# Optimization experiments

Hardware: AMD Instinct MI355X
Metric: run time of the kernel (lower is better)

## Reference

```python
import jax, jax.numpy as jnp
import numpy as np

B, M, EMBED, HEADS = 64, 1024, 1024, 8
HD = EMBED // HEADS  # 128
MID = 64             # att_mid_dim[1]
ALPHA = 1.3          # cfg.MODEL.BILINEAR.ELU_ALPHA (CELU)


def celu(x):
    return jax.nn.celu(x, alpha=ALPHA)


def group_norm(x, w, b, G=HEADS, eps=1e-5):
    # torch GroupNorm in source uses unbiased variance (ddof=1)
    N, C = x.shape
    xg = x.reshape(N, G, C // G)
    m = xg.mean(-1, keepdims=True)
    v = xg.var(-1, ddof=1, keepdims=True)
    xg = (xg - m) / jnp.sqrt(v + eps)
    return xg.reshape(N, C) * w + b


def setup_inputs() -> dict:
    key = jax.random.key(0)
    ks = jax.random.split(key, 16)
    s = 0.02
    return {
        "h_state": jax.random.normal(ks[0], (B, EMBED), jnp.float32),
        "att_feats": jax.random.normal(ks[1], (B, M, EMBED), jnp.float32),
        "att_mask": jnp.ones((B, M), jnp.float32),
        "p_att_feats": jax.random.normal(ks[2], (B, M, 2 * EMBED), jnp.float32),
        "Wq": jax.random.normal(ks[3], (EMBED, EMBED), jnp.float32) * s,
        "bq": jnp.zeros((EMBED,), jnp.float32),
        "gnw_q": jnp.ones((EMBED,), jnp.float32),
        "gnb_q": jnp.zeros((EMBED,), jnp.float32),
        "Wv1": jax.random.normal(ks[4], (EMBED, EMBED), jnp.float32) * s,
        "bv1": jnp.zeros((EMBED,), jnp.float32),
        "gnw_v1": jnp.ones((EMBED,), jnp.float32),
        "gnb_v1": jnp.zeros((EMBED,), jnp.float32),
        "Wb": jax.random.normal(ks[5], (HEADS, HD, MID), jnp.float32) * s,
        "bb": jax.random.normal(ks[6], (HEADS, MID), jnp.float32) * s,
        "Ws": jax.random.normal(ks[7], (HEADS, MID, 1), jnp.float32) * s,
        "bs": jax.random.normal(ks[8], (HEADS, 1), jnp.float32) * s,
        "Wc": jax.random.normal(ks[9], (HEADS, MID, HD), jnp.float32) * s,
        "bc": jax.random.normal(ks[10], (HEADS, HD), jnp.float32) * s,
        "Wt": jax.random.normal(ks[11], (2 * EMBED, EMBED), jnp.float32) * s,
        "bt": jnp.zeros((EMBED,), jnp.float32),
        "lnw": jnp.ones((EMBED,), jnp.float32),
        "lnb": jnp.zeros((EMBED,), jnp.float32),
    }


def reference(h_state, att_feats, att_mask, p_att_feats,
              Wq, bq, gnw_q, gnb_q, Wv1, bv1, gnw_v1, gnb_v1,
              Wb, bb, Ws, bs, Wc, bc, Wt, bt, lnw, lnb):
    b = h_state.shape[0]
    # precompute=True path: split p_att_feats into key / value2
    p_key = p_att_feats[..., :EMBED]
    p_value2 = p_att_feats[..., EMBED:]

    # q / v1 branches: Linear -> CELU -> GroupNorm
    q = group_norm(celu(h_state @ Wq + bq), gnw_q, gnb_q)    # [B, E]
    v1 = group_norm(celu(h_state @ Wv1 + bv1), gnw_v1, gnb_v1)

    p_query = q.reshape(b, HEADS, HD)[:, :, None, :]          # [B, H, 1, D]
    p_value1 = v1.reshape(b, HEADS, HD)[:, :, None, :]        # [B, H, 1, D]
    p_key = p_key.reshape(b, M, HEADS, HD).transpose(0, 2, 1, 3)     # [B, H, M, D]
    p_value2 = p_value2.reshape(b, M, HEADS, HD).transpose(0, 2, 1, 3)

    fusion = p_value2 * p_value1                              # [B, H, M, D]
    att_map = p_query * p_key                                 # [B, H, M, D]

    # attention_basic: MH_Linear + ReLU (dropout is identity at eval)
    am = jax.nn.relu(jnp.einsum('bhmi,hio->bhmo', att_map, Wb) + bb[None, :, None, :])  # [B,H,M,MID]

    mask = att_mask[:, None, :]                               # [B, 1, M]
    mext = mask[..., None]                                    # [B, 1, M, 1]
    att_map_pool = (am * mext).sum(-2) / mext.sum(-2)         # [B, H, MID]

    alpha_spatial = (jnp.einsum('bhmi,hio->bhmo', am, Ws) + bs[None, :, None, :])[..., 0]  # [B,H,M]
    alpha_spatial = jnp.where(mask == 0, -1e9, alpha_spatial)
    alpha_spatial = jax.nn.softmax(alpha_spatial, axis=-1)

    att = jnp.einsum('bhm,bhmd->bhd', alpha_spatial, fusion)  # [B, H, D]

    alpha_channel = jax.nn.sigmoid(jnp.einsum('bhi,hio->bho', att_map_pool, Wc) + bc[None])
    att = (att * alpha_channel).reshape(b, EMBED)

    out = jnp.concatenate([h_state, att], axis=-1) @ Wt + bt  # [B, E]
    mu = out.mean(-1, keepdims=True)
    var = out.var(-1, keepdims=True)
    out = (out - mu) / jnp.sqrt(var + 1e-5) * lnw + lnb
    return out
```

## Files before the change

### kernel.cpp

```cpp
#include <hip/hip_runtime.h>
#include <hip/hip_bf16.h>
#include <cmath>

#define NB 64
#define NM 1024
#define NE 1024
#define NH 8
#define NHD 128
#define NMID 64
#define CELU_ALPHA 1.3f

typedef __attribute__((ext_vector_type(8))) short bf16x8;
typedef __attribute__((ext_vector_type(4))) float f32x4;

__device__ __forceinline__ float celuf(float x) {
    return x > 0.f ? x : CELU_ALPHA * expm1f(x / CELU_ALPHA);
}

__device__ __forceinline__ short f2bf(float x) {
    __hip_bfloat16 b = __float2bfloat16(x);
    return *reinterpret_cast<short*>(&b);
}

__global__ __launch_bounds__(256) void a1_tile(
    const float* __restrict__ h, const float* __restrict__ Wq,
    const float* __restrict__ Wv1, float* __restrict__ partA)
{
    const int t = threadIdx.x;
    const int mat = blockIdx.x >> 7;
    const int kq = (blockIdx.x >> 4) & 7;
    const int cc = (blockIdx.x & 15) * 64;
    const int kbase = kq * 128;
    const float* __restrict__ W = mat ? Wv1 : Wq;

    __shared__ float wl[128][64];
    __shared__ float hl[64][132];

#pragma unroll
    for (int u = 0; u < 8; ++u) {
        const int f = t + 256 * u;
        const int row = f >> 4, c4 = f & 15;
        *(float4*)&wl[row][c4 * 4] =
            *(const float4*)&W[(size_t)(kbase + row) * 1024 + cc + c4 * 4];
    }
#pragma unroll
    for (int u = 0; u < 8; ++u) {
        const int f = t + 256 * u;
        const int r = f >> 5, k4 = f & 31;
        *(float4*)&hl[r][k4 * 4] = *(const float4*)&h[r * 1024 + kbase + k4 * 4];
    }
    __syncthreads();

    const int r0 = (t >> 4) * 4;
    const int c0 = (t & 15) * 4;
    float acc[4][4];
#pragma unroll
    for (int i = 0; i < 4; ++i)
#pragma unroll
        for (int j = 0; j < 4; ++j) acc[i][j] = 0.f;

#pragma unroll 4
    for (int k = 0; k < 128; ++k) {
        const float4 w4 = *(const float4*)&wl[k][c0];
        const float h0 = hl[r0][k], h1 = hl[r0 + 1][k];
        const float h2 = hl[r0 + 2][k], h3 = hl[r0 + 3][k];
        acc[0][0] = fmaf(h0, w4.x, acc[0][0]); acc[0][1] = fmaf(h0, w4.y, acc[0][1]);
        acc[0][2] = fmaf(h0, w4.z, acc[0][2]); acc[0][3] = fmaf(h0, w4.w, acc[0][3]);
        acc[1][0] = fmaf(h1, w4.x, acc[1][0]); acc[1][1] = fmaf(h1, w4.y, acc[1][1]);
        acc[1][2] = fmaf(h1, w4.z, acc[1][2]); acc[1][3] = fmaf(h1, w4.w, acc[1][3]);
        acc[2][0] = fmaf(h2, w4.x, acc[2][0]); acc[2][1] = fmaf(h2, w4.y, acc[2][1]);
        acc[2][2] = fmaf(h2, w4.z, acc[2][2]); acc[2][3] = fmaf(h2, w4.w, acc[2][3]);
        acc[3][0] = fmaf(h3, w4.x, acc[3][0]); acc[3][1] = fmaf(h3, w4.y, acc[3][1]);
        acc[3][2] = fmaf(h3, w4.z, acc[3][2]); acc[3][3] = fmaf(h3, w4.w, acc[3][3]);
    }

    float* __restrict__ out = partA + (size_t)(mat * 8 + kq) * 65536;
#pragma unroll
    for (int i = 0; i < 4; ++i) {
        float4 v = {acc[i][0], acc[i][1], acc[i][2], acc[i][3]};
        *(float4*)&out[(r0 + i) * 1024 + cc + c0] = v;
    }
}

__global__ __launch_bounds__(256) void a2b0(
    const float* __restrict__ partA,
    const float* __restrict__ bq, const float* __restrict__ bv1,
    const float* __restrict__ gnw_q, const float* __restrict__ gnb_q,
    const float* __restrict__ gnw_v, const float* __restrict__ gnb_v,
    const float* __restrict__ Wb,
    float* __restrict__ v1buf, short* __restrict__ wbq_g)
{
    const int bid = blockIdx.x;
    const int b = bid >> 3, hh = bid & 7;
    const int t = threadIdx.x;
    const int mat = t >> 7;
    const int c = t & 127;
    const int ch = hh * 128 + c;
    const int w = t >> 6, lane = t & 63;

    __shared__ float q_lds[128];
    __shared__ float red[4][2];
    __shared__ float wb_l[128][68];

#pragma unroll
    for (int u = 0; u < 8; ++u) {
        const int f = t + 256 * u;
        const int i = f >> 4, o4 = f & 15;
        *(float4*)&wb_l[i][o4 * 4] = *(const float4*)&Wb[hh * 8192 + i * 64 + o4 * 4];
    }

    float x = mat ? bv1[ch] : bq[ch];
#pragma unroll
    for (int kq = 0; kq < 8; ++kq)
        x += partA[(size_t)(mat * 8 + kq) * 65536 + b * 1024 + ch];
    x = celuf(x);

    float s = x, s2 = x * x;
#pragma unroll
    for (int m = 32; m >= 1; m >>= 1) {
        s += __shfl_xor(s, m);
        s2 += __shfl_xor(s2, m);
    }
    if (lane == 0) { red[w][0] = s; red[w][1] = s2; }
    __syncthreads();
    const float S  = red[mat * 2][0] + red[mat * 2 + 1][0];
    const float S2 = red[mat * 2][1] + red[mat * 2 + 1][1];
    const float mean = S * (1.f / 128.f);
    const float var = (S2 - 128.f * mean * mean) * (1.f / 127.f);
    const float inv = rsqrtf(var + 1e-5f);
    const float gw = mat ? gnw_v[ch] : gnw_q[ch];
    const float gb = mat ? gnb_v[ch] : gnb_q[ch];
    const float y = (x - mean) * inv * gw + gb;
    if (mat == 0) q_lds[c] = y;
    else v1buf[b * 1024 + ch] = y;
    __syncthreads();

    const int o = t & 63;
    const int i0 = (t >> 6) * 32;
    union { short sv[32]; uint4 q4[4]; } u;
#pragma unroll 8
    for (int v = 0; v < 32; ++v) {
        const int i = i0 + v;
        u.sv[v] = f2bf(q_lds[i] * wb_l[i][o]);
    }
    uint4* dst = (uint4*)&wbq_g[(size_t)bid * 8192 + o * 128 + i0];
#pragma unroll
    for (int r = 0; r < 4; ++r) dst[r] = u.q4[r];
}

__global__ __launch_bounds__(256) void b_fused(
    const float* __restrict__ pat, const float* __restrict__ mask,
    const short* __restrict__ wbq_g,
    const float* __restrict__ bb, const float* __restrict__ Ws,
    const float* __restrict__ bs,
    float* __restrict__ pool_pt, float* __restrict__ esum_pt,
    float* __restrict__ av_pt)
{
    const int t = threadIdx.x;
    const int bid = blockIdx.x;
    const int b = bid >> 5;
    const int chunk = (bid >> 3) & 3;
    const int h = bid & 7;
    const int sidx = (((b << 3) | h) << 2) | chunk;
    const int w = t >> 6;
    const int lane = t & 63;
    const int ln15 = lane & 15;
    const int lg = lane >> 4;
    const int dg = lane & 31;
    const int rwg = lane >> 5;

    __shared__ float mask_lds[256];
    __shared__ float e_lds[4][16];
    __shared__ float att_red[4][128];
    __shared__ float pool_red[4][64];
    __shared__ float esum_red[4];

    mask_lds[t] = mask[b * 1024 + chunk * 256 + t];

    const short* __restrict__ wb = wbq_g + (size_t)(sidx >> 2) * 8192;
    bf16x8 bfr[4][4];
#pragma unroll
    for (int nt = 0; nt < 4; ++nt)
#pragma unroll
        for (int ks = 0; ks < 4; ++ks)
            bfr[nt][ks] = *(const bf16x8*)&wb[(nt * 16 + ln15) * 128 + ks * 32 + lg * 8];

    float wsr[4], bbr[4];
#pragma unroll
    for (int nt = 0; nt < 4; ++nt) {
        wsr[nt] = Ws[h * 64 + nt * 16 + ln15];
        bbr[nt] = bb[h * 64 + nt * 16 + ln15];
    }
    const float bsh = bs[h];
    float pool_part[4] = {0.f, 0.f, 0.f, 0.f};
    float esum_part = 0.f;
    float4 a4 = {0.f, 0.f, 0.f, 0.f};

    const float* __restrict__ patk = pat + (size_t)b * NM * 2048 + h * 128;
    const float* __restrict__ patv = patk + 1024;

    __syncthreads();

    for (int it = 0; it < 4; ++it) {
        const int ml0 = (w * 4 + it) * 16;
        const int m0 = chunk * 256 + ml0;

        const float* __restrict__ rowp = patk + (size_t)(m0 + ln15) * 2048 + lg * 8;
        float4 ax[4], ay[4];
#pragma unroll
        for (int ks = 0; ks < 4; ++ks) {
            ax[ks] = *(const float4*)(rowp + ks * 32);
            ay[ks] = *(const float4*)(rowp + ks * 32 + 4);
        }

        bf16x8 af[4];
#pragma unroll
        for (int ks = 0; ks < 4; ++ks) {
            union { bf16x8 v; short s[8]; } u8;
            u8.s[0] = f2bf(ax[ks].x); u8.s[1] = f2bf(ax[ks].y);
            u8.s[2] = f2bf(ax[ks].z); u8.s[3] = f2bf(ax[ks].w);
            u8.s[4] = f2bf(ay[ks].x); u8.s[5] = f2bf(ay[ks].y);
            u8.s[6] = f2bf(ay[ks].z); u8.s[7] = f2bf(ay[ks].w);
            af[ks] = u8.v;
        }

        f32x4 acc[4];
#pragma unroll
        for (int nt = 0; nt < 4; ++nt) acc[nt] = (f32x4){0.f, 0.f, 0.f, 0.f};
#pragma unroll
        for (int ks = 0; ks < 4; ++ks)
#pragma unroll
            for (int nt = 0; nt < 4; ++nt)
                acc[nt] = __builtin_amdgcn_mfma_f32_16x16x32_bf16(af[ks], bfr[nt][ks], acc[nt], 0, 0, 0);

#pragma unroll
        for (int j = 0; j < 4; ++j) {
            const int ml = ml0 + lg * 4 + j;
            const float mk = mask_lds[ml];
            float sp = 0.f;
#pragma unroll
            for (int nt = 0; nt < 4; ++nt) {
                float a = acc[nt][j] + bbr[nt];
                a = fmaxf(a, 0.f);
                sp = fmaf(a, wsr[nt], sp);
                pool_part[nt] = fmaf(a, mk, pool_part[nt]);
            }
            sp += __shfl_xor(sp, 1);
            sp += __shfl_xor(sp, 2);
            sp += __shfl_xor(sp, 4);
            sp += __shfl_xor(sp, 8);
            if (ln15 == 0) {
                const float e = (mk == 0.f) ? 0.f : expf(sp + bsh);
                e_lds[w][lg * 4 + j] = e;
                esum_part += e;
            }
        }

        const float* __restrict__ vrow = patv + (size_t)(m0 + rwg) * 2048 + dg * 4;
#pragma unroll 8
        for (int r = 0; r < 8; ++r) {
            const float4 v = *(const float4*)(vrow + (size_t)(2 * r) * 2048);
            const float e = e_lds[w][rwg + 2 * r];
            a4.x = fmaf(e, v.x, a4.x);
            a4.y = fmaf(e, v.y, a4.y);
            a4.z = fmaf(e, v.z, a4.z);
            a4.w = fmaf(e, v.w, a4.w);
        }
    }

    a4.x += __shfl_xor(a4.x, 32);
    a4.y += __shfl_xor(a4.y, 32);
    a4.z += __shfl_xor(a4.z, 32);
    a4.w += __shfl_xor(a4.w, 32);
    if (lane < 32) *(float4*)&att_red[w][dg * 4] = a4;

#pragma unroll
    for (int nt = 0; nt < 4; ++nt) {
        float p = pool_part[nt];
        p += __shfl_xor(p, 16);
        p += __shfl_xor(p, 32);
        if (lane < 16) pool_red[w][nt * 16 + lane] = p;
    }

#pragma unroll
    for (int m = 32; m >= 1; m >>= 1) esum_part += __shfl_xor(esum_part, m);
    if (lane == 0) esum_red[w] = esum_part;
    __syncthreads();

    if (t < 128)
        av_pt[(size_t)sidx * 128 + t] =
            att_red[0][t] + att_red[1][t] + att_red[2][t] + att_red[3][t];
    else if (t < 192)
        pool_pt[(size_t)sidx * 64 + (t - 128)] =
            pool_red[0][t - 128] + pool_red[1][t - 128] + pool_red[2][t - 128] + pool_red[3][t - 128];
    else if (t == 192)
        esum_pt[sidx] = esum_red[0] + esum_red[1] + esum_red[2] + esum_red[3];
}

__global__ __launch_bounds__(256) void b5_final(
    const float* __restrict__ pool_pt, const float* __restrict__ esum_pt,
    const float* __restrict__ av_pt, const float* __restrict__ mask,
    const float* __restrict__ Wc, const float* __restrict__ bc,
    const float* __restrict__ v1, float* __restrict__ att_out)
{
    const int t = threadIdx.x;
    const int bid = blockIdx.x;
    const int b = bid >> 3;
    const int h = bid & 7;
    const int w = t >> 6, lane = t & 63;

    __shared__ float red4[4];
    __shared__ float pool2[64];

    const float4 mk4 = *(const float4*)&mask[b * 1024 + t * 4];
    float msp = mk4.x + mk4.y + mk4.z + mk4.w;
#pragma unroll
    for (int m = 32; m >= 1; m >>= 1) msp += __shfl_xor(msp, m);
    if (lane == 0) red4[w] = msp;
    __syncthreads();
    const float msum = red4[0] + red4[1] + red4[2] + red4[3];

    if (t < 64) {
        const float pp = pool_pt[(size_t)(bid * 4) * 64 + t] + pool_pt[(size_t)(bid * 4 + 1) * 64 + t]
                       + pool_pt[(size_t)(bid * 4 + 2) * 64 + t] + pool_pt[(size_t)(bid * 4 + 3) * 64 + t];
        pool2[t] = pp / msum;
    }
    __syncthreads();

    if (t < 128) {
        const int d = t;
        const float av = av_pt[(size_t)(bid * 4) * 128 + d] + av_pt[(size_t)(bid * 4 + 1) * 128 + d]
                       + av_pt[(size_t)(bid * 4 + 2) * 128 + d] + av_pt[(size_t)(bid * 4 + 3) * 128 + d];
        const float esum = esum_pt[bid * 4] + esum_pt[bid * 4 + 1]
                         + esum_pt[bid * 4 + 2] + esum_pt[bid * 4 + 3];
        const float att = av / esum;
        float ac = bc[h * 128 + d];
#pragma unroll 8
        for (int o = 0; o < 64; ++o)
            ac = fmaf(pool2[o], Wc[h * 8192 + o * 128 + d], ac);
        const float sig = 1.f / (1.f + expf(-ac));
        att_out[b * 1024 + h * 128 + d] = att * sig * v1[b * 1024 + h * 128 + d];
    }
}

__global__ __launch_bounds__(256) void c1_tile(
    const float* __restrict__ h, const float* __restrict__ att,
    const float* __restrict__ Wt, float* __restrict__ part)
{
    const int t = threadIdx.x;
    const int kq = blockIdx.x >> 4;
    const int cc = (blockIdx.x & 15) * 64;
    const float* __restrict__ x = (kq < 8) ? h : att;
    const int kbase = (kq & 7) * 128;

    __shared__ float wl[128][64];
    __shared__ float hl[64][132];

#pragma unroll
    for (int u = 0; u < 8; ++u) {
        const int f = t + 256 * u;
        const int row = f >> 4, c4 = f & 15;
        *(float4*)&wl[row][c4 * 4] =
            *(const float4*)&Wt[(size_t)(kq * 128 + row) * 1024 + cc + c4 * 4];
    }
#pragma unroll
    for (int u = 0; u < 8; ++u) {
        const int f = t + 256 * u;
        const int r = f >> 5, k4 = f & 31;
        *(float4*)&hl[r][k4 * 4] = *(const float4*)&x[r * 1024 + kbase + k4 * 4];
    }
    __syncthreads();

    const int r0 = (t >> 4) * 4;
    const int c0 = (t & 15) * 4;
    float acc[4][4];
#pragma unroll
    for (int i = 0; i < 4; ++i)
#pragma unroll
        for (int j = 0; j < 4; ++j) acc[i][j] = 0.f;

#pragma unroll 4
    for (int k = 0; k < 128; ++k) {
        const float4 w4 = *(const float4*)&wl[k][c0];
        const float h0 = hl[r0][k], h1 = hl[r0 + 1][k];
        const float h2 = hl[r0 + 2][k], h3 = hl[r0 + 3][k];
        acc[0][0] = fmaf(h0, w4.x, acc[0][0]); acc[0][1] = fmaf(h0, w4.y, acc[0][1]);
        acc[0][2] = fmaf(h0, w4.z, acc[0][2]); acc[0][3] = fmaf(h0, w4.w, acc[0][3]);
        acc[1][0] = fmaf(h1, w4.x, acc[1][0]); acc[1][1] = fmaf(h1, w4.y, acc[1][1]);
        acc[1][2] = fmaf(h1, w4.z, acc[1][2]); acc[1][3] = fmaf(h1, w4.w, acc[1][3]);
        acc[2][0] = fmaf(h2, w4.x, acc[2][0]); acc[2][1] = fmaf(h2, w4.y, acc[2][1]);
        acc[2][2] = fmaf(h2, w4.z, acc[2][2]); acc[2][3] = fmaf(h2, w4.w, acc[2][3]);
        acc[3][0] = fmaf(h3, w4.x, acc[3][0]); acc[3][1] = fmaf(h3, w4.y, acc[3][1]);
        acc[3][2] = fmaf(h3, w4.z, acc[3][2]); acc[3][3] = fmaf(h3, w4.w, acc[3][3]);
    }

#pragma unroll
    for (int i = 0; i < 4; ++i) {
        float4 v = {acc[i][0], acc[i][1], acc[i][2], acc[i][3]};
        *(float4*)&part[(size_t)kq * 65536 + (r0 + i) * 1024 + cc + c0] = v;
    }
}

__global__ __launch_bounds__(256) void c2_ln(
    const float* __restrict__ part, const float* __restrict__ bt,
    const float* __restrict__ lnw, const float* __restrict__ lnb,
    float* __restrict__ out)
{
    const int t = threadIdx.x;
    const int row = blockIdx.x;
    const int w = t >> 6, lane = t & 63;
    __shared__ float red[4];

    float4 v = *(const float4*)&bt[t * 4];
#pragma unroll
    for (int qd = 0; qd < 16; ++qd) {
        const float4 p = *(const float4*)&part[(size_t)qd * 65536 + row * 1024 + t * 4];
        v.x += p.x; v.y += p.y; v.z += p.z; v.w += p.w;
    }
    float s = v.x + v.y + v.z + v.w;
#pragma unroll
    for (int m = 32; m >= 1; m >>= 1) s += __shfl_xor(s, m);
    if (lane == 0) red[w] = s;
    __syncthreads();
    const float mean = (red[0] + red[1] + red[2] + red[3]) * (1.f / 1024.f);
    __syncthreads();
    const float d0 = v.x - mean, d1 = v.y - mean, d2 = v.z - mean, d3 = v.w - mean;
    float ss = d0 * d0 + d1 * d1 + d2 * d2 + d3 * d3;
#pragma unroll
    for (int m = 32; m >= 1; m >>= 1) ss += __shfl_xor(ss, m);
    if (lane == 0) red[w] = ss;
    __syncthreads();
    const float var = (red[0] + red[1] + red[2] + red[3]) * (1.f / 1024.f);
    const float inv = rsqrtf(var + 1e-5f);
    const float4 w4 = *(const float4*)&lnw[t * 4];
    const float4 b4 = *(const float4*)&lnb[t * 4];
    float4 y;
    y.x = d0 * inv * w4.x + b4.x;
    y.y = d1 * inv * w4.y + b4.y;
    y.z = d2 * inv * w4.z + b4.z;
    y.w = d3 * inv * w4.w + b4.w;
    *(float4*)&out[row * 1024 + t * 4] = y;
}

extern "C" void kernel_launch(void* const* d_in, const int* in_sizes, int n_in,
                              void* d_out, int out_size, void* d_ws, size_t ws_size,
                              hipStream_t stream)
{
    const float* h_state  = (const float*)d_in[0];
    const float* att_mask = (const float*)d_in[2];
    const float* pat      = (const float*)d_in[3];
    const float* Wq       = (const float*)d_in[4];
    const float* bq       = (const float*)d_in[5];
    const float* gnw_q    = (const float*)d_in[6];
    const float* gnb_q    = (const float*)d_in[7];
    const float* Wv1      = (const float*)d_in[8];
    const float* bv1      = (const float*)d_in[9];
    const float* gnw_v1   = (const float*)d_in[10];
    const float* gnb_v1   = (const float*)d_in[11];
    const float* Wb       = (const float*)d_in[12];
    const float* bb       = (const float*)d_in[13];
    const float* Ws       = (const float*)d_in[14];
    const float* bs       = (const float*)d_in[15];
    const float* Wc       = (const float*)d_in[16];
    const float* bc       = (const float*)d_in[17];
    const float* Wt       = (const float*)d_in[18];
    const float* bt       = (const float*)d_in[19];
    const float* lnw      = (const float*)d_in[20];
    const float* lnb      = (const float*)d_in[21];
    float* out = (float*)d_out;

    float* ws      = (float*)d_ws;
    float* v1buf   = ws;
    float* attb    = ws + 65536;
    float* parts   = ws + 131072;
    short* wbq_g   = (short*)(ws + 1179648);
    float* pool_pt = ws + 3276800;
    float* esum_pt = ws + 3407872;
    float* av_pt   = ws + 3409920;

    a1_tile<<<256, 256, 0, stream>>>(h_state, Wq, Wv1, parts);
    a2b0<<<512, 256, 0, stream>>>(parts, bq, bv1, gnw_q, gnb_q, gnw_v1, gnb_v1,
                                  Wb, v1buf, wbq_g);
    b_fused<<<2048, 256, 0, stream>>>(pat, att_mask, wbq_g, bb, Ws, bs,
                                      pool_pt, esum_pt, av_pt);
    b5_final<<<512, 256, 0, stream>>>(pool_pt, esum_pt, av_pt, att_mask,
                                      Wc, bc, v1buf, attb);
    c1_tile<<<256, 256, 0, stream>>>(h_state, attb, Wt, parts);
    c2_ln<<<64, 256, 0, stream>>>(parts, bt, lnw, lnb, out);
}
```

Before: 162.2 us.

## Fuse final attention reduction into b_fused via last-block atomic, halve GEMM K-split

Removes the b5_final kernel. The last of the four chunk blocks for each (batch, head) now finishes the reduction inside b_fused, using a threadfence plus an atomic counter that a2b0 resets. Separately, the K-split of the two small GEMMs (a1_tile, c1_tile) is halved to 64 per block, which doubles the block count to 512 and doubles the number of partial buffers the reducers must sum. This saves one launch and aims for more parallelism on the GEMMs, at the cost of extra partial-sum traffic and serialized tail work.

```diff
diff --git a/kernel.cpp b/kernel.cpp
--- a/kernel.cpp
+++ b/kernel.cpp
@@ -27,26 +27,26 @@
     const float* __restrict__ Wv1, float* __restrict__ partA)
 {
     const int t = threadIdx.x;
-    const int mat = blockIdx.x >> 7;
-    const int kq = (blockIdx.x >> 4) & 7;
+    const int mat = blockIdx.x >> 8;
+    const int kq = (blockIdx.x >> 4) & 15;
     const int cc = (blockIdx.x & 15) * 64;
-    const int kbase = kq * 128;
+    const int kbase = kq * 64;
     const float* __restrict__ W = mat ? Wv1 : Wq;
 
-    __shared__ float wl[128][64];
-    __shared__ float hl[64][132];
-
-#pragma unroll
-    for (int u = 0; u < 8; ++u) {
+    __shared__ float wl[64][64];
+    __shared__ float hl[64][68];
+
+#pragma unroll
+    for (int u = 0; u < 4; ++u) {
         const int f = t + 256 * u;
         const int row = f >> 4, c4 = f & 15;
         *(float4*)&wl[row][c4 * 4] =
             *(const float4*)&W[(size_t)(kbase + row) * 1024 + cc + c4 * 4];
     }
 #pragma unroll
-    for (int u = 0; u < 8; ++u) {
+    for (int u = 0; u < 4; ++u) {
         const int f = t + 256 * u;
-        const int r = f >> 5, k4 = f & 31;
+        const int r = f >> 4, k4 = f & 15;
         *(float4*)&hl[r][k4 * 4] = *(const float4*)&h[r * 1024 + kbase + k4 * 4];
     }
     __syncthreads();
@@ -60,7 +60,7 @@
         for (int j = 0; j < 4; ++j) acc[i][j] = 0.f;
 
 #pragma unroll 4
-    for (int k = 0; k < 128; ++k) {
+    for (int k = 0; k < 64; ++k) {
         const float4 w4 = *(const float4*)&wl[k][c0];
         const float h0 = hl[r0][k], h1 = hl[r0 + 1][k];
         const float h2 = hl[r0 + 2][k], h3 = hl[r0 + 3][k];
@@ -74,7 +74,7 @@
         acc[3][2] = fmaf(h3, w4.z, acc[3][2]); acc[3][3] = fmaf(h3, w4.w, acc[3][3]);
     }
 
-    float* __restrict__ out = partA + (size_t)(mat * 8 + kq) * 65536;
+    float* __restrict__ out = partA + (size_t)(mat * 16 + kq) * 65536;
 #pragma unroll
     for (int i = 0; i < 4; ++i) {
         float4 v = {acc[i][0], acc[i][1], acc[i][2], acc[i][3]};
@@ -88,7 +88,8 @@
     const float* __restrict__ gnw_q, const float* __restrict__ gnb_q,
     const float* __restrict__ gnw_v, const float* __restrict__ gnb_v,
     const float* __restrict__ Wb,
-    float* __restrict__ v1buf, short* __restrict__ wbq_g)
+    float* __restrict__ v1buf, short* __restrict__ wbq_g,
+    int* __restrict__ cnt)
 {
     const int bid = blockIdx.x;
     const int b = bid >> 3, hh = bid & 7;
@@ -102,6 +103,8 @@
     __shared__ float red[4][2];
     __shared__ float wb_l[128][68];
 
+    if (t == 0) cnt[bid] = 0;
+
 #pragma unroll
     for (int u = 0; u < 8; ++u) {
         const int f = t + 256 * u;
@@ -111,8 +114,8 @@
 
     float x = mat ? bv1[ch] : bq[ch];
 #pragma unroll
-    for (int kq = 0; kq < 8; ++kq)
-        x += partA[(size_t)(mat * 8 + kq) * 65536 + b * 1024 + ch];
+    for (int kq = 0; kq < 16; ++kq)
+        x += partA[(size_t)(mat * 16 + kq) * 65536 + b * 1024 + ch];
     x = celuf(x);
 
     float s = x, s2 = x * x;
@@ -153,8 +156,11 @@
     const short* __restrict__ wbq_g,
     const float* __restrict__ bb, const float* __restrict__ Ws,
     const float* __restrict__ bs,
+    const float* __restrict__ Wc, const float* __restrict__ bc,
+    const float* __restrict__ v1,
     float* __restrict__ pool_pt, float* __restrict__ esum_pt,
-    float* __restrict__ av_pt)
+    float* __restrict__ msum_pt, float* __restrict__ av_pt,
+    int* __restrict__ cnt, float* __restrict__ att_out)
 {
     const int t = threadIdx.x;
     const int bid = blockIdx.x;
@@ -174,8 +180,19 @@
     __shared__ float att_red[4][128];
     __shared__ float pool_red[4][64];
     __shared__ float esum_red[4];
-
-    mask_lds[t] = mask[b * 1024 + chunk * 256 + t];
+    __shared__ float msum_red[4];
+    __shared__ float fin_pool2[64];
+    __shared__ float fin_se[2];
+    __shared__ int   fin_flag;
+
+    const float mk0 = mask[b * 1024 + chunk * 256 + t];
+    mask_lds[t] = mk0;
+    {
+        float msp = mk0;
+#pragma unroll
+        for (int m = 32; m >= 1; m >>= 1) msp += __shfl_xor(msp, m);
+        if (lane == 0) msum_red[w] = msp;
+    }
 
     const short* __restrict__ wb = wbq_g + (size_t)(sidx >> 2) * 8192;
     bf16x8 bfr[4][4];
@@ -295,49 +312,41 @@
             pool_red[0][t - 128] + pool_red[1][t - 128] + pool_red[2][t - 128] + pool_red[3][t - 128];
     else if (t == 192)
         esum_pt[sidx] = esum_red[0] + esum_red[1] + esum_red[2] + esum_red[3];
-}
-
-__global__ __launch_bounds__(256) void b5_final(
-    const float* __restrict__ pool_pt, const float* __restrict__ esum_pt,
-    const float* __restrict__ av_pt, const float* __restrict__ mask,
-    const float* __restrict__ Wc, const float* __restrict__ bc,
-    const float* __restrict__ v1, float* __restrict__ att_out)
-{
-    const int t = threadIdx.x;
-    const int bid = blockIdx.x;
-    const int b = bid >> 3;
-    const int h = bid & 7;
-    const int w = t >> 6, lane = t & 63;
-
-    __shared__ float red4[4];
-    __shared__ float pool2[64];
-
-    const float4 mk4 = *(const float4*)&mask[b * 1024 + t * 4];
-    float msp = mk4.x + mk4.y + mk4.z + mk4.w;
-#pragma unroll
-    for (int m = 32; m >= 1; m >>= 1) msp += __shfl_xor(msp, m);
-    if (lane == 0) red4[w] = msp;
-    __syncthreads();
-    const float msum = red4[0] + red4[1] + red4[2] + red4[3];
-
-    if (t < 64) {
-        const float pp = pool_pt[(size_t)(bid * 4) * 64 + t] + pool_pt[(size_t)(bid * 4 + 1) * 64 + t]
-                       + pool_pt[(size_t)(bid * 4 + 2) * 64 + t] + pool_pt[(size_t)(bid * 4 + 3) * 64 + t];
-        pool2[t] = pp / msum;
-    }
+    else if (t == 193)
+        msum_pt[sidx] = msum_red[0] + msum_red[1] + msum_red[2] + msum_red[3];
+
+    __threadfence();
+    if (t == 0) {
+        const int old = atomicAdd(&cnt[sidx >> 2], 1);
+        fin_flag = (old == 3);
+    }
+    __syncthreads();
+    if (!fin_flag) return;
+
+    __threadfence();
+    const int bh = sidx >> 2;
+    if (t == 64) {
+        fin_se[0] = esum_pt[bh * 4] + esum_pt[bh * 4 + 1]
+                  + esum_pt[bh * 4 + 2] + esum_pt[bh * 4 + 3];
+        fin_se[1] = msum_pt[bh * 4] + msum_pt[bh * 4 + 1]
+                  + msum_pt[bh * 4 + 2] + msum_pt[bh * 4 + 3];
+    }
+    if (t < 64)
+        fin_pool2[t] = pool_pt[(size_t)(bh * 4) * 64 + t] + pool_pt[(size_t)(bh * 4 + 1) * 64 + t]
+                     + pool_pt[(size_t)(bh * 4 + 2) * 64 + t] + pool_pt[(size_t)(bh * 4 + 3) * 64 + t];
+    __syncthreads();
+    if (t < 64) fin_pool2[t] /= fin_se[1];
     __syncthreads();
 
     if (t < 128) {
         const int d = t;
-        const float av = av_pt[(size_t)(bid * 4) * 128 + d] + av_pt[(size_t)(bid * 4 + 1) * 128 + d]
-                       + av_pt[(size_t)(bid * 4 + 2) * 128 + d] + av_pt[(size_t)(bid * 4 + 3) * 128 + d];
-        const float esum = esum_pt[bid * 4] + esum_pt[bid * 4 + 1]
-                         + esum_pt[bid * 4 + 2] + esum_pt[bid * 4 + 3];
-        const float att = av / esum;
+        const float av = av_pt[(size_t)(bh * 4) * 128 + d] + av_pt[(size_t)(bh * 4 + 1) * 128 + d]
+                       + av_pt[(size_t)(bh * 4 + 2) * 128 + d] + av_pt[(size_t)(bh * 4 + 3) * 128 + d];
+        const float att = av / fin_se[0];
         float ac = bc[h * 128 + d];
 #pragma unroll 8
         for (int o = 0; o < 64; ++o)
-            ac = fmaf(pool2[o], Wc[h * 8192 + o * 128 + d], ac);
+            ac = fmaf(fin_pool2[o], Wc[h * 8192 + o * 128 + d], ac);
         const float sig = 1.f / (1.f + expf(-ac));
         att_out[b * 1024 + h * 128 + d] = att * sig * v1[b * 1024 + h * 128 + d];
     }
@@ -350,23 +359,23 @@
     const int t = threadIdx.x;
     const int kq = blockIdx.x >> 4;
     const int cc = (blockIdx.x & 15) * 64;
-    const float* __restrict__ x = (kq < 8) ? h : att;
-    const int kbase = (kq & 7) * 128;
-
-    __shared__ float wl[128][64];
-    __shared__ float hl[64][132];
-
-#pragma unroll
-    for (int u = 0; u < 8; ++u) {
+    const float* __restrict__ x = (kq < 16) ? h : att;
+    const int kbase = (kq & 15) * 64;
+
+    __shared__ float wl[64][64];
+    __shared__ float hl[64][68];
+
+#pragma unroll
+    for (int u = 0; u < 4; ++u) {
         const int f = t + 256 * u;
         const int row = f >> 4, c4 = f & 15;
         *(float4*)&wl[row][c4 * 4] =
-            *(const float4*)&Wt[(size_t)(kq * 128 + row) * 1024 + cc + c4 * 4];
-    }
-#pragma unroll
-    for (int u = 0; u < 8; ++u) {
+            *(const float4*)&Wt[(size_t)(kq * 64 + row) * 1024 + cc + c4 * 4];
+    }
+#pragma unroll
+    for (int u = 0; u < 4; ++u) {
         const int f = t + 256 * u;
-        const int r = f >> 5, k4 = f & 31;
+        const int r = f >> 4, k4 = f & 15;
         *(float4*)&hl[r][k4 * 4] = *(const float4*)&x[r * 1024 + kbase + k4 * 4];
     }
     __syncthreads();
@@ -380,7 +389,7 @@
         for (int j = 0; j < 4; ++j) acc[i][j] = 0.f;
 
 #pragma unroll 4
-    for (int k = 0; k < 128; ++k) {
+    for (int k = 0; k < 64; ++k) {
         const float4 w4 = *(const float4*)&wl[k][c0];
         const float h0 = hl[r0][k], h1 = hl[r0 + 1][k];
         const float h2 = hl[r0 + 2][k], h3 = hl[r0 + 3][k];
@@ -413,7 +422,7 @@
 
     float4 v = *(const float4*)&bt[t * 4];
 #pragma unroll
-    for (int qd = 0; qd < 16; ++qd) {
+    for (int qd = 0; qd < 32; ++qd) {
         const float4 p = *(const float4*)&part[(size_t)qd * 65536 + row * 1024 + t * 4];
         v.x += p.x; v.y += p.y; v.z += p.z; v.w += p.w;
     }
@@ -473,18 +482,20 @@
     float* v1buf   = ws;
     float* attb    = ws + 65536;
     float* parts   = ws + 131072;
-    short* wbq_g   = (short*)(ws + 1179648);
-    float* pool_pt = ws + 3276800;
-    float* esum_pt = ws + 3407872;
-    float* av_pt   = ws + 3409920;
-
-    a1_tile<<<256, 256, 0, stream>>>(h_state, Wq, Wv1, parts);
+    short* wbq_g   = (short*)(ws + 2228224);
+    float* pool_pt = ws + 4325376;
+    float* esum_pt = ws + 4456448;
+    float* msum_pt = ws + 4458496;
+    float* av_pt   = ws + 4460544;
+    int*   cnt     = (int*)(ws + 4722688);
+
+    a1_tile<<<512, 256, 0, stream>>>(h_state, Wq, Wv1, parts);
     a2b0<<<512, 256, 0, stream>>>(parts, bq, bv1, gnw_q, gnb_q, gnw_v1, gnb_v1,
-                                  Wb, v1buf, wbq_g);
+                                  Wb, v1buf, wbq_g, cnt);
     b_fused<<<2048, 256, 0, stream>>>(pat, att_mask, wbq_g, bb, Ws, bs,
-                                      pool_pt, esum_pt, av_pt);
-    b5_final<<<512, 256, 0, stream>>>(pool_pt, esum_pt, av_pt, att_mask,
-                                      Wc, bc, v1buf, attb);
-    c1_tile<<<256, 256, 0, stream>>>(h_state, attb, Wt, parts);
+                                      Wc, bc, v1buf,
+                                      pool_pt, esum_pt, msum_pt, av_pt,
+                                      cnt, attb);
+    c1_tile<<<512, 256, 0, stream>>>(h_state, attb, Wt, parts);
     c2_ln<<<64, 256, 0, stream>>>(parts, bt, lnw, lnb, out);
 }
```

New measurement: 608.6 us. 3.75x slower.
